# Kernel tuning notes

Measured on AMD Instinct MI355X. Metric: run time of the kernel, lower is better.

Reference implementation:

```python
import jax, jax.numpy as jnp
import numpy as np

B, D, UNITS, NW = 64, 2048, 1024, 64  # batch, input_dim, units, n_weights


def _build_hash_indices(rng):
    """Replicates hash_matrix(): for each (unit j, bucket k), the (1-shifted)
    input positions i with hash(i,j) == k, padded with 0 (-> zero column)."""
    indx = rng.integers(0, NW, size=(D, UNITS))  # hash of (i, j) into [0, NW)
    counts = np.zeros((UNITS, NW), dtype=np.int64)
    for k in range(NW):
        counts[:, k] = (indx == k).sum(axis=0)
    L = int(counts.max())
    out = np.zeros((UNITS, NW, L), dtype=np.int64)
    for j in range(UNITS):
        col = indx[:, j]
        order = np.argsort(col, kind='stable')
        cnts = np.bincount(col, minlength=NW)
        splits = np.cumsum(cnts)[:-1]
        for k, part in enumerate(np.split(order, splits)):
            out[j, k, :len(part)] = part + 1  # +1 shift; 0 = padding
    return out


def setup_inputs() -> dict:
    key = jax.random.key(0)
    kx, kw = jax.random.split(key)
    x = jax.random.normal(kx, (B, D), dtype=jnp.float32)
    w = jax.random.normal(kw, (NW,), dtype=jnp.float32) * 0.05  # random_normal_initializer
    b = jnp.zeros((UNITS,), dtype=jnp.float32)
    indices = jnp.asarray(_build_hash_indices(np.random.default_rng(2)))
    return {"x": x, "w": w, "b": b, "indices": indices}


def reference(x, w, b, indices):
    # prepend a zero column so padding index 0 gathers 0.0
    x_cat = jnp.pad(x, ((0, 0), (1, 0)))                 # [B, D+1]
    gathered = jnp.take(x_cat, indices, axis=1)          # [B, UNITS, NW, L]
    reduced = gathered.sum(axis=-1)                      # [B, UNITS, NW]
    return jnp.einsum('buk,k->bu', reduced, w) + b       # [B, UNITS]
```

## Files before the change

kernel.cpp:

```cpp
#include <hip/hip_runtime.h>


#define B_DIM   64
#define D_DIM   2048
#define UNITS_N 1024
#define NW_N    64
#define U_PER_BLOCK 4
#define THREADS 512

__global__ __launch_bounds__(THREADS)
void EfficientHashedLinear_72043781423546_kernel(
    const float* __restrict__ x,
    const float* __restrict__ w,
    const float* __restrict__ bias,
    const int*   __restrict__ indices,
    float*       __restrict__ out,
    int L, int NWL)
{
    __shared__ float rows[U_PER_BLOCK][D_DIM];
    __shared__ float w_lds[NW_N];

    const int tid = threadIdx.x;
    const int u0  = blockIdx.x * U_PER_BLOCK;

    #pragma unroll
    for (int i = tid; i < U_PER_BLOCK * D_DIM; i += THREADS)
        ((float*)rows)[i] = 0.0f;
    if (tid < NW_N) w_lds[tid] = w[tid];
    __syncthreads();

    const int total = U_PER_BLOCK * NWL;
    const int base  = u0 * NWL;
    for (int e = tid; e < total; e += THREADS) {
        int uu  = e / NWL;
        int r   = e - uu * NWL;
        int k   = r / L;
        int idx = indices[base + e];
        if (idx > 0) rows[uu][idx - 1] = w_lds[k];
    }
    __syncthreads();

    const int wave = tid >> 6;
    const int lane = tid & 63;
    const int b0   = wave * 8;

    float acc[8][U_PER_BLOCK];
    #pragma unroll
    for (int bj = 0; bj < 8; ++bj)
        #pragma unroll
        for (int uu = 0; uu < U_PER_BLOCK; ++uu)
            acc[bj][uu] = 0.0f;

    #pragma unroll 4
    for (int step = 0; step < D_DIM / 64; ++step) {
        const int i = lane + step * 64;
        float rv[U_PER_BLOCK];
        #pragma unroll
        for (int uu = 0; uu < U_PER_BLOCK; ++uu)
            rv[uu] = rows[uu][i];
        #pragma unroll
        for (int bj = 0; bj < 8; ++bj) {
            float xv = x[(b0 + bj) * D_DIM + i];
            #pragma unroll
            for (int uu = 0; uu < U_PER_BLOCK; ++uu)
                acc[bj][uu] += xv * rv[uu];
        }
    }

    #pragma unroll
    for (int bj = 0; bj < 8; ++bj) {
        #pragma unroll
        for (int uu = 0; uu < U_PER_BLOCK; ++uu) {
            float v = acc[bj][uu];
            #pragma unroll
            for (int off = 32; off > 0; off >>= 1)
                v += __shfl_down(v, off, 64);
            if (lane == 0)
                out[(b0 + bj) * UNITS_N + (u0 + uu)] = v + bias[u0 + uu];
        }
    }
}

extern "C" void kernel_launch(void* const* d_in, const int* in_sizes, int n_in,
                              void* d_out, int out_size, void* d_ws, size_t ws_size,
                              hipStream_t stream) {
    const float* x       = (const float*)d_in[0];
    const float* w       = (const float*)d_in[1];
    const float* bias    = (const float*)d_in[2];
    const int*   indices = (const int*)d_in[3];
    float*       out     = (float*)d_out;

    const int L   = in_sizes[3] / (UNITS_N * NW_N);
    const int NWL = NW_N * L;

    dim3 grid(UNITS_N / U_PER_BLOCK);
    dim3 block(THREADS);
    EfficientHashedLinear_72043781423546_kernel<<<grid, block, 0, stream>>>(
        x, w, bias, indices, out, L, NWL);
}
```

Measured before the change: 96.84 us.

## Vectorize loads with float4, restructure scatter per bucket, double block threads

Doubles the threads per block to 1024 so each wave handles 4 batch rows instead of 8. The index scatter is reorganized so each wave walks (unit, bucket) pairs, which removes the per-element divides. LDS zeroing, LDS row reads and x reads now use float4 vectors, and the inner loop is fully unrolled. The aim is wider memory transactions and more waves in flight. The cost is higher register pressure under 1024-thread launch bounds, and the scatter loop leaves lanes idle when L is small.

```diff
diff --git a/kernel.cpp b/kernel.cpp
--- a/kernel.cpp
+++ b/kernel.cpp
@@ -3,10 +3,11 @@
 
 #define B_DIM   64
 #define D_DIM   2048
+#define D4      (D_DIM / 4)
 #define UNITS_N 1024
 #define NW_N    64
 #define U_PER_BLOCK 4
-#define THREADS 512
+#define THREADS 1024
 
 __global__ __launch_bounds__(THREADS)
 void EfficientHashedLinear_72043781423546_kernel(
@@ -15,60 +16,72 @@
     const float* __restrict__ bias,
     const int*   __restrict__ indices,
     float*       __restrict__ out,
-    int L, int NWL)
+    int L)
 {
     __shared__ float rows[U_PER_BLOCK][D_DIM];
     __shared__ float w_lds[NW_N];
 
-    const int tid = threadIdx.x;
-    const int u0  = blockIdx.x * U_PER_BLOCK;
+    const int tid  = threadIdx.x;
+    const int wave = tid >> 6;
+    const int lane = tid & 63;
+    const int u0   = blockIdx.x * U_PER_BLOCK;
 
-    #pragma unroll
-    for (int i = tid; i < U_PER_BLOCK * D_DIM; i += THREADS)
-        ((float*)rows)[i] = 0.0f;
-    if (tid < NW_N) w_lds[tid] = w[tid];
-    __syncthreads();
-
-    const int total = U_PER_BLOCK * NWL;
-    const int base  = u0 * NWL;
-    for (int e = tid; e < total; e += THREADS) {
-        int uu  = e / NWL;
-        int r   = e - uu * NWL;
-        int k   = r / L;
-        int idx = indices[base + e];
-        if (idx > 0) rows[uu][idx - 1] = w_lds[k];
+    {
+        float4* r4 = (float4*)rows;
+        const float4 z = make_float4(0.f, 0.f, 0.f, 0.f);
+        #pragma unroll
+        for (int i = tid; i < U_PER_BLOCK * D4; i += THREADS)
+            r4[i] = z;
+        if (tid < NW_N) w_lds[tid] = w[tid];
     }
     __syncthreads();
 
-    const int wave = tid >> 6;
-    const int lane = tid & 63;
-    const int b0   = wave * 8;
+    #pragma unroll 4
+    for (int p = 0; p < 16; ++p) {
+        const int pair = wave * 16 + p;
+        const int uu   = pair >> 6;
+        const int k    = pair & 63;
+        const int* bp  = indices + ((size_t)(u0 + uu) * NW_N + k) * L;
+        const float wk = w_lds[k];
+        for (int l = lane; l < L; l += 64) {
+            int idx = bp[l];
+            if (idx > 0) rows[uu][idx - 1] = wk;
+        }
+    }
+    __syncthreads();
 
-    float acc[8][U_PER_BLOCK];
+    const int b0 = wave * 4;
+    const float4* x4 = (const float4*)x;
+
+    float acc[4][U_PER_BLOCK];
     #pragma unroll
-    for (int bj = 0; bj < 8; ++bj)
+    for (int bj = 0; bj < 4; ++bj)
         #pragma unroll
         for (int uu = 0; uu < U_PER_BLOCK; ++uu)
             acc[bj][uu] = 0.0f;
 
-    #pragma unroll 4
-    for (int step = 0; step < D_DIM / 64; ++step) {
-        const int i = lane + step * 64;
-        float rv[U_PER_BLOCK];
+    #pragma unroll
+    for (int step = 0; step < D4 / 64; ++step) {
+        const int i4 = step * 64 + lane;
+        float4 rv[U_PER_BLOCK];
         #pragma unroll
         for (int uu = 0; uu < U_PER_BLOCK; ++uu)
-            rv[uu] = rows[uu][i];
+            rv[uu] = ((const float4*)rows[uu])[i4];
         #pragma unroll
-        for (int bj = 0; bj < 8; ++bj) {
-            float xv = x[(b0 + bj) * D_DIM + i];
+        for (int bj = 0; bj < 4; ++bj) {
+            const float4 xv = x4[(b0 + bj) * D4 + i4];
             #pragma unroll
-            for (int uu = 0; uu < U_PER_BLOCK; ++uu)
-                acc[bj][uu] += xv * rv[uu];
+            for (int uu = 0; uu < U_PER_BLOCK; ++uu) {
+                acc[bj][uu] += xv.x * rv[uu].x;
+                acc[bj][uu] += xv.y * rv[uu].y;
+                acc[bj][uu] += xv.z * rv[uu].z;
+                acc[bj][uu] += xv.w * rv[uu].w;
+            }
         }
     }
 
     #pragma unroll
-    for (int bj = 0; bj < 8; ++bj) {
+    for (int bj = 0; bj < 4; ++bj) {
         #pragma unroll
         for (int uu = 0; uu < U_PER_BLOCK; ++uu) {
             float v = acc[bj][uu];
@@ -90,11 +103,10 @@
     const int*   indices = (const int*)d_in[3];
     float*       out     = (float*)d_out;
 
-    const int L   = in_sizes[3] / (UNITS_N * NW_N);
-    const int NWL = NW_N * L;
+    const int L = in_sizes[3] / (UNITS_N * NW_N);
 
     dim3 grid(UNITS_N / U_PER_BLOCK);
     dim3 block(THREADS);
     EfficientHashedLinear_72043781423546_kernel<<<grid, block, 0, stream>>>(
-        x, w, bias, indices, out, L, NWL);
+        x, w, bias, indices, out, L);
 }
```

New measurement: 165.8 us. 71.2% more time.
